# Kernel optimization log

Hardware: AMD Instinct MI355X
Metric: run time of the kernel (lower is better)

The kernel has to match this reference:

```python
import jax, jax.numpy as jnp
import numpy as np

B, C, H, W = 64, 16, 64, 64
NET = 16          # SpatialNN.net_size
S = C - 1         # number of SpatialNN steps in the ModuleList
LOG_2PI = float(np.log(2.0 * np.pi))


def _log_normal(x, loc, log_scale):
    # Normal(loc, exp(log_scale)).log_prob(x)
    z = (x - loc) * jnp.exp(-log_scale)
    return -0.5 * z * z - log_scale - 0.5 * LOG_2PI


def setup_inputs() -> dict:
    key = jax.random.key(0)
    ks = jax.random.split(key, 14)
    sc = 0.1
    samples = jax.random.normal(ks[0], (B, C, H, W), jnp.float32)
    n1_w1 = sc * jax.random.normal(ks[1], (NET, 1), jnp.float32)
    n1_b1 = sc * jax.random.normal(ks[2], (NET,), jnp.float32)
    n1_w2 = sc * jax.random.normal(ks[3], (NET, NET), jnp.float32)
    n1_b2 = sc * jax.random.normal(ks[4], (NET,), jnp.float32)
    n1_w3 = sc * jax.random.normal(ks[5], (2, NET), jnp.float32)
    n1_b3 = sc * jax.random.normal(ks[6], (2,), jnp.float32)
    # step s (s=0..S-1) consumes samples[:, :s+1]; pad conv1 weight to C input
    # channels with zeros in columns > s (identical math, enables fusion)
    w1 = sc * jax.random.normal(ks[7], (S, NET, C), jnp.float32)
    tri = (jnp.arange(C)[None, None, :] <= jnp.arange(S)[:, None, None]).astype(jnp.float32)
    w1 = w1 * tri
    b1 = sc * jax.random.normal(ks[8], (S, NET), jnp.float32)
    w2 = sc * jax.random.normal(ks[9], (S, NET, NET), jnp.float32)
    b2 = sc * jax.random.normal(ks[10], (S, NET), jnp.float32)
    w3 = sc * jax.random.normal(ks[11], (S, 2, NET), jnp.float32)
    b3 = sc * jax.random.normal(ks[12], (S, 2), jnp.float32)
    return {"samples": samples,
            "n1_w1": n1_w1, "n1_b1": n1_b1, "n1_w2": n1_w2, "n1_b2": n1_b2,
            "n1_w3": n1_w3, "n1_b3": n1_b3,
            "w1": w1, "b1": b1, "w2": w2, "b2": b2, "w3": w3, "b3": b3}


def reference(samples, n1_w1, n1_b1, n1_w2, n1_b2, n1_w3, n1_b3,
              w1, b1, w2, b2, w3, b3):
    # --- first channel: n1 applied to a zeros input (as in the torch code) ---
    x0 = jnp.zeros_like(samples[:, :1])                       # [B,1,H,W]
    h = jax.nn.relu(jnp.einsum('oc,bchw->bohw', n1_w1, x0) + n1_b1[:, None, None])
    h = jax.nn.relu(jnp.einsum('op,bphw->bohw', n1_w2, h) + n1_b2[:, None, None])
    p1 = jnp.einsum('op,bphw->bohw', n1_w3, h) + n1_b3[:, None, None]   # [B,2,H,W]
    lp1 = _log_normal(samples[:, 0], p1[:, 0], p1[:, 1])      # [B,H,W]

    h = jax.nn.relu(jnp.einsum('soc,bchw->bsohw', w1, samples)
                    + b1[None, :, :, None, None])             # [B,S,16,H,W]
    h = jax.nn.relu(jnp.einsum('sop,bsphw->bsohw', w2, h)
                    + b2[None, :, :, None, None])
    p = jnp.einsum('sop,bsphw->bsohw', w3, h) + b3[None, :, :, None, None]  # [B,S,2,H,W]
    lps = _log_normal(samples[:, 1:], p[:, :, 0], p[:, :, 1])  # [B,S,H,W]

    return lp1 + jnp.sum(lps, axis=1)                          # [B,H,W]
```

## Files before the change

### kernel.cpp

```cpp
#include <hip/hip_runtime.h>


#define NEG_HALF_LOG_2PI -0.91893853320467274f

typedef _Float16 f16x4 __attribute__((ext_vector_type(4)));
typedef __fp16   hf2   __attribute__((ext_vector_type(2)));
typedef float    f32x4 __attribute__((ext_vector_type(4)));

__device__ inline f16x4 pack_f16(f32x4 v) {
    hf2 p0 = __builtin_amdgcn_cvt_pkrtz(v[0], v[1]);
    hf2 p1 = __builtin_amdgcn_cvt_pkrtz(v[2], v[3]);
    f16x4 r;
    __builtin_memcpy(&r, &p0, 4);
    __builtin_memcpy((char*)&r + 4, &p1, 4);
    return r;
}

__device__ inline f16x4 relu_pack(f32x4 d) {
    hf2 p0 = __builtin_amdgcn_cvt_pkrtz(d[0], d[1]);
    hf2 p1 = __builtin_amdgcn_cvt_pkrtz(d[2], d[3]);
    f16x4 r;
    __builtin_memcpy(&r, &p0, 4);
    __builtin_memcpy((char*)&r + 4, &p1, 4);
    const f16x4 z = {(_Float16)0, (_Float16)0, (_Float16)0, (_Float16)0};
    return __builtin_elementwise_max(r, z);
}

__global__ __launch_bounds__(256, 4) void spatial_main(
    const float* __restrict__ samples,
    const float* __restrict__ n1_b1,
    const float* __restrict__ n1_w2,
    const float* __restrict__ n1_b2,
    const float* __restrict__ n1_w3,
    const float* __restrict__ n1_b3,
    const float* __restrict__ w1,
    const float* __restrict__ b1,
    const float* __restrict__ w2,
    const float* __restrict__ b2,
    const float* __restrict__ w3,
    const float* __restrict__ b3,
    float* __restrict__ out)
{
    __shared__ _Float16 fA[45 * 256];
    __shared__ float    fC[15 * 2 * 16];

    const int tid   = threadIdx.x;
    const int lane  = tid & 63;
    const int wv    = tid >> 6;
    const int q     = lane >> 4;
    const int col   = lane & 15;
    const int lane4 = lane << 2;
    const int q4    = q << 2;
    const int roff  = col * 16 + q4;

    for (int j = tid; j < 30 * 64; j += 256) {
        int m   = j >> 6;
        int rem = j & 63;
        int r   = rem >> 2;
        int c   = rem & 3;
        const float* src = (m < 15) ? (w1 + m * 256) : (w2 + (m - 15) * 256);
        f32x4 v = *(const f32x4*)(src + r * 16 + (c << 2));
        int sl = (m < 15) ? (m * 3) : ((m - 15) * 3 + 1);
        *(f16x4*)&fA[sl * 256 + (((c << 4) + r) << 2)] = pack_f16(v);
    }
    for (int j = tid; j < 15 * 64; j += 256) {
        int s  = j >> 6;
        int ln = j & 63;
        int r  = ln & 15;
        int qq = ln >> 4;
        f32x4 v = {0.f, 0.f, 0.f, 0.f};
        if ((r & 3) < 2) v = *(const f32x4*)(w3 + s * 32 + ((r & 1) << 4) + (qq << 2));
        *(f16x4*)&fA[(s * 3 + 2) * 256 + (ln << 2)] = pack_f16(v);
    }
    for (int j = tid; j < 15 * 2 * 16; j += 256) {
        int s = j >> 5, layer = (j >> 4) & 1, o = j & 15;
        fC[j] = layer ? b2[s * 16 + o] : b1[s * 16 + o];
    }

    const int pbase = blockIdx.x * 256 + wv * 64;
    const int b     = pbase >> 12;
    const int hw    = pbase & 4095;
    const float* xw = samples + ((size_t)b << 16) + hw;

    f16x4 bx[4];
    #pragma unroll
    for (int ch = 0; ch < 4; ++ch)
        #pragma unroll
        for (int i = 0; i < 4; ++i)
            bx[ch][i] = (_Float16)xw[((q4 + i) << 12) + (ch << 4) + col];

    float xs[16];
    #pragma unroll
    for (int c = 0; c < 16; ++c)
        xs[c] = xw[(c << 12) + lane];

    float accz, accl;
    {
        f32x4 c1h = *(const f32x4*)(n1_b1 + q4);
        f16x4 h1h = relu_pack(c1h);
        f16x4 a2h = pack_f16(*(const f32x4*)(n1_w2 + roff));
        f32x4 c2h = *(const f32x4*)(n1_b2 + q4);
        f32x4 d2h = __builtin_amdgcn_mfma_f32_16x16x16f16(a2h, h1h, c2h, 0, 0, 0);
        f16x4 h2h = relu_pack(d2h);
        f32x4 v3h = {0.f, 0.f, 0.f, 0.f};
        if ((col & 3) < 2) v3h = *(const f32x4*)(n1_w3 + ((col & 1) << 4) + q4);
        f16x4 a3h = pack_f16(v3h);
        f32x4 c3h = {n1_b3[0], n1_b3[1], 0.0f, 0.0f};
        f32x4 d3h = __builtin_amdgcn_mfma_f32_16x16x16f16(a3h, h2h, c3h, 0, 0, 0);
        float ls = d3h[1];
        float z0 = (xs[0] - d3h[0]) * __expf(-ls);
        accz = z0 * z0;
        accl = ls;
    }

    __syncthreads();

    f16x4 a1c = *(const f16x4*)&fA[0 * 256 + lane4];
    f16x4 a2c = *(const f16x4*)&fA[1 * 256 + lane4];
    f16x4 a3c = *(const f16x4*)&fA[2 * 256 + lane4];
    f32x4 c1c = *(const f32x4*)&fC[0 * 16 + q4];
    f32x4 c2c = *(const f32x4*)&fC[1 * 16 + q4];

    #pragma unroll
    for (int s = 0; s < 15; ++s) {
        f16x4 a1n, a2n, a3n;
        f32x4 c1n, c2n;
        if (s < 14) {
            a1n = *(const f16x4*)&fA[((s + 1) * 3 + 0) * 256 + lane4];
            a2n = *(const f16x4*)&fA[((s + 1) * 3 + 1) * 256 + lane4];
            a3n = *(const f16x4*)&fA[((s + 1) * 3 + 2) * 256 + lane4];
            c1n = *(const f32x4*)&fC[((s + 1) * 2 + 0) * 16 + q4];
            c2n = *(const f32x4*)&fC[((s + 1) * 2 + 1) * 16 + q4];
        }
        f32x4 c3 = {b3[s * 2 + 0], b3[s * 2 + 1], 0.0f, 0.0f};

        f32x4 d1[4];
        #pragma unroll
        for (int ch = 0; ch < 4; ++ch)
            d1[ch] = __builtin_amdgcn_mfma_f32_16x16x16f16(a1c, bx[ch], c1c, 0, 0, 0);
        f16x4 h1[4];
        #pragma unroll
        for (int ch = 0; ch < 4; ++ch)
            h1[ch] = relu_pack(d1[ch]);
        f32x4 d2[4];
        #pragma unroll
        for (int ch = 0; ch < 4; ++ch)
            d2[ch] = __builtin_amdgcn_mfma_f32_16x16x16f16(a2c, h1[ch], c2c, 0, 0, 0);
        f16x4 h2[4];
        #pragma unroll
        for (int ch = 0; ch < 4; ++ch)
            h2[ch] = relu_pack(d2[ch]);
        f32x4 d3[4];
        #pragma unroll
        for (int ch = 0; ch < 4; ++ch)
            d3[ch] = __builtin_amdgcn_mfma_f32_16x16x16f16(a3c, h2[ch], c3, 0, 0, 0);

        float loc = q == 0 ? d3[0][0] : q == 1 ? d3[1][0] : q == 2 ? d3[2][0] : d3[3][0];
        float ls  = q == 0 ? d3[0][1] : q == 1 ? d3[1][1] : q == 2 ? d3[2][1] : d3[3][1];
        float z   = (xs[s + 1] - loc) * __expf(-ls);
        accz = fmaf(z, z, accz);
        accl += ls;

        a1c = a1n; a2c = a2n; a3c = a3n; c1c = c1n; c2c = c2n;
    }

    out[pbase + lane] = fmaf(-0.5f, accz, 16.0f * NEG_HALF_LOG_2PI - accl);
}

extern "C" void kernel_launch(void* const* d_in, const int* in_sizes, int n_in,
                              void* d_out, int out_size, void* d_ws, size_t ws_size,
                              hipStream_t stream) {
    const float* samples = (const float*)d_in[0];
    const float* n1_b1   = (const float*)d_in[2];
    const float* n1_w2   = (const float*)d_in[3];
    const float* n1_b2   = (const float*)d_in[4];
    const float* n1_w3   = (const float*)d_in[5];
    const float* n1_b3   = (const float*)d_in[6];
    const float* w1      = (const float*)d_in[7];
    const float* b1      = (const float*)d_in[8];
    const float* w2      = (const float*)d_in[9];
    const float* b2      = (const float*)d_in[10];
    const float* w3      = (const float*)d_in[11];
    const float* b3      = (const float*)d_in[12];
    float* out = (float*)d_out;

    spatial_main<<<dim3(1024), dim3(256), 0, stream>>>(
        samples, n1_b1, n1_w2, n1_b2, n1_w3, n1_b3,
        w1, b1, w2, b2, w3, b3, out);
}
```

Before: 96.90 us.

## Double block size and issue weight loads after sample loads

Blocks grow from 256 to 512 threads (eight waves, 512 pixels each) and the grid halves, so each block's shared-memory weight staging is spread over more pixels. The weight, bias and head-weight global loads now go into registers after the sample loads have been issued, and the LDS writes follow, so global latency for samples and weights can overlap. The costs are higher register pressure from the staging registers and fewer, larger blocks, which may lower occupancy or leave the tail imbalanced.

New measurement: 95.32 us, median of 2. No clear change (-1.6%).

```diff
diff --git a/kernel.cpp b/kernel.cpp
--- a/kernel.cpp
+++ b/kernel.cpp
@@ -26,7 +26,7 @@
     return __builtin_elementwise_max(r, z);
 }
 
-__global__ __launch_bounds__(256, 4) void spatial_main(
+__global__ __launch_bounds__(512, 4) void spatial_main(
     const float* __restrict__ samples,
     const float* __restrict__ n1_b1,
     const float* __restrict__ n1_w2,
@@ -53,31 +53,7 @@
     const int q4    = q << 2;
     const int roff  = col * 16 + q4;
 
-    for (int j = tid; j < 30 * 64; j += 256) {
-        int m   = j >> 6;
-        int rem = j & 63;
-        int r   = rem >> 2;
-        int c   = rem & 3;
-        const float* src = (m < 15) ? (w1 + m * 256) : (w2 + (m - 15) * 256);
-        f32x4 v = *(const f32x4*)(src + r * 16 + (c << 2));
-        int sl = (m < 15) ? (m * 3) : ((m - 15) * 3 + 1);
-        *(f16x4*)&fA[sl * 256 + (((c << 4) + r) << 2)] = pack_f16(v);
-    }
-    for (int j = tid; j < 15 * 64; j += 256) {
-        int s  = j >> 6;
-        int ln = j & 63;
-        int r  = ln & 15;
-        int qq = ln >> 4;
-        f32x4 v = {0.f, 0.f, 0.f, 0.f};
-        if ((r & 3) < 2) v = *(const f32x4*)(w3 + s * 32 + ((r & 1) << 4) + (qq << 2));
-        *(f16x4*)&fA[(s * 3 + 2) * 256 + (ln << 2)] = pack_f16(v);
-    }
-    for (int j = tid; j < 15 * 2 * 16; j += 256) {
-        int s = j >> 5, layer = (j >> 4) & 1, o = j & 15;
-        fC[j] = layer ? b2[s * 16 + o] : b1[s * 16 + o];
-    }
-
-    const int pbase = blockIdx.x * 256 + wv * 64;
+    const int pbase = blockIdx.x * 512 + wv * 64;
     const int b     = pbase >> 12;
     const int hw    = pbase & 4095;
     const float* xw = samples + ((size_t)b << 16) + hw;
@@ -93,6 +69,62 @@
     #pragma unroll
     for (int c = 0; c < 16; ++c)
         xs[c] = xw[(c << 12) + lane];
+
+    f32x4 t1[4];
+    #pragma unroll
+    for (int i = 0; i < 4; ++i) {
+        int j = tid + i * 512;
+        if (j < 1920) {
+            int m   = j >> 6;
+            int rem = j & 63;
+            int r   = rem >> 2;
+            int c   = rem & 3;
+            const float* src = (m < 15) ? (w1 + m * 256) : (w2 + (m - 15) * 256);
+            t1[i] = *(const f32x4*)(src + r * 16 + (c << 2));
+        }
+    }
+    f32x4 t2[2];
+    #pragma unroll
+    for (int i = 0; i < 2; ++i) {
+        int j = tid + i * 512;
+        t2[i] = f32x4{0.f, 0.f, 0.f, 0.f};
+        if (j < 960) {
+            int s  = j >> 6;
+            int ln = j & 63;
+            int r  = ln & 15;
+            int qq = ln >> 4;
+            if ((r & 3) < 2)
+                t2[i] = *(const f32x4*)(w3 + s * 32 + ((r & 1) << 4) + (qq << 2));
+        }
+    }
+    float t3 = 0.f;
+    if (tid < 480) {
+        int s = tid >> 5, layer = (tid >> 4) & 1, o = tid & 15;
+        t3 = layer ? b2[s * 16 + o] : b1[s * 16 + o];
+    }
+
+    #pragma unroll
+    for (int i = 0; i < 4; ++i) {
+        int j = tid + i * 512;
+        if (j < 1920) {
+            int m   = j >> 6;
+            int rem = j & 63;
+            int r   = rem >> 2;
+            int c   = rem & 3;
+            int sl  = (m < 15) ? (m * 3) : ((m - 15) * 3 + 1);
+            *(f16x4*)&fA[sl * 256 + (((c << 4) + r) << 2)] = pack_f16(t1[i]);
+        }
+    }
+    #pragma unroll
+    for (int i = 0; i < 2; ++i) {
+        int j = tid + i * 512;
+        if (j < 960) {
+            int s  = j >> 6;
+            int ln = j & 63;
+            *(f16x4*)&fA[(s * 3 + 2) * 256 + (ln << 2)] = pack_f16(t2[i]);
+        }
+    }
+    if (tid < 480) fC[tid] = t3;
 
     float accz, accl;
     {
@@ -184,7 +216,7 @@
     const float* b3      = (const float*)d_in[12];
     float* out = (float*)d_out;
 
-    spatial_main<<<dim3(1024), dim3(256), 0, stream>>>(
+    spatial_main<<<dim3(512), dim3(512), 0, stream>>>(
         samples, n1_b1, n1_w2, n1_b2, n1_w3, n1_b3,
         w1, b1, w2, b2, w3, b3, out);
 }
```
